# Kernel tuning notes

Measured on AMD Instinct MI355X. Metric: run time of the kernel, lower is better.

The kernel has to match this reference:

```python
import jax, jax.numpy as jnp
from jax import lax
import numpy as np

B = 256
EMB_DIM = 64
N_EMB = 512
LAT1 = 1024   # 16 slots * 64
LAT2 = 512
LAT = LAT1 + LAT2  # 1536
COMMIT = 0.25
EMB_COST = 1.0


def setup_inputs() -> dict:
    key = jax.random.key(0)
    ks = iter(jax.random.split(key, 40))

    def w(shape, fan_in):
        return jax.random.normal(next(ks), shape, jnp.float32) * np.float32(1.0 / np.sqrt(fan_in))

    def b(n):
        return jax.random.normal(next(ks), (n,), jnp.float32) * np.float32(0.01)

    inp = {}
    inp['x'] = jax.random.normal(next(ks), (B, 3, 64, 64), jnp.float32)
    # encoder convs, torch OIHW layout, k=4
    inp['ew0'] = w((64, 3, 4, 4), 3 * 16);   inp['eb0'] = b(64)
    inp['ew1'] = w((64, 64, 4, 4), 64 * 16); inp['eb1'] = b(64)
    inp['ew2'] = w((128, 64, 4, 4), 64 * 16); inp['eb2'] = b(128)
    inp['ew3'] = w((256, 128, 4, 4), 128 * 16); inp['eb3'] = b(256)
    # encoder fc11: 4096 -> 1024 -> 1024 -> 1536, stored (in,out)
    inp['fw0'] = w((4096, 1024), 4096); inp['fb0'] = b(1024)
    inp['fw1'] = w((1024, 1024), 1024); inp['fb1'] = b(1024)
    inp['fw2'] = w((1024, LAT), 1024);  inp['fb2'] = b(LAT)
    # VQ codebook
    inp['codebook'] = jax.random.normal(next(ks), (N_EMB, EMB_DIM), jnp.float32)
    # decoder fc3: 1536 -> 512 -> 1024 -> 4096
    inp['gw0'] = w((LAT, 512), LAT);    inp['gb0'] = b(512)
    inp['gw1'] = w((512, 1024), 512);   inp['gb1'] = b(1024)
    inp['gw2'] = w((1024, 4096), 1024); inp['gb2'] = b(4096)
    # decoder ConvTranspose2d weights, torch layout (Cin, Cout, kh, kw)
    inp['tw0'] = w((256, 128, 4, 4), 256 * 16); inp['tb0'] = b(128)
    inp['tw1'] = w((128, 64, 4, 4), 128 * 16);  inp['tb1'] = b(64)
    inp['tw2'] = w((64, 64, 4, 4), 64 * 16);    inp['tb2'] = b(64)
    inp['tw3'] = w((64, 3, 4, 4), 64 * 16);     inp['tb3'] = b(3)
    return inp


def _conv(x, w, b):
    # Conv2d k=4 s=2 p=1 -> halves H,W
    y = lax.conv_general_dilated(x, w, (2, 2), ((1, 1), (1, 1)),
                                 dimension_numbers=('NCHW', 'OIHW', 'NCHW'))
    return y + b[None, :, None, None]


def _convt(x, w, b):
    # ConvTranspose2d k=4 s=2 p=1 -> doubles H,W.
    # Equivalent to lhs_dilation=2, pad k-1-p=2, flipped kernel, swapped I/O.
    wf = jnp.flip(w, (2, 3)).transpose(1, 0, 2, 3)
    y = lax.conv_general_dilated(x, wf, (1, 1), ((2, 2), (2, 2)),
                                 lhs_dilation=(2, 2),
                                 dimension_numbers=('NCHW', 'OIHW', 'NCHW'))
    return y + b[None, :, None, None]


def _forward(x, ew0, eb0, ew1, eb1, ew2, eb2, ew3, eb3,
             fw0, fb0, fw1, fb1, fw2, fb2, codebook,
             gw0, gb0, gw1, gb1, gw2, gb2,
             tw0, tb0, tw1, tb1, tw2, tb2, tw3, tb3):
    relu = jax.nn.relu
    # --- encoder conv stack (last conv has no ReLU) ---
    h = relu(_conv(x, ew0, eb0))
    h = relu(_conv(h, ew1, eb1))
    h = relu(_conv(h, ew2, eb2))
    h = _conv(h, ew3, eb3)                      # [B,256,4,4]
    h = h.reshape(h.shape[0], -1)               # [B,4096]
    h = relu(h @ fw0 + fb0)
    h = relu(h @ fw1 + fb1)
    z = h @ fw2 + fb2                           # [B,1536]
    # --- split content / style (isVQStyle=False) ---
    z_c = z[:, :LAT1]
    z_s = z[:, LAT1:]
    # --- vector quantize z_c (16 slots of dim 64, shared codebook) ---
    flat = z_c.reshape(-1, EMB_DIM)             # [B*16, 64]
    d = (jnp.sum(flat * flat, axis=1, keepdims=True)
         + jnp.sum(codebook * codebook, axis=1)
         - 2.0 * flat @ codebook.T)             # [B*16, 512]
    idx = jnp.argmin(d, axis=1)
    quantized = codebook[idx].reshape(z_c.shape)  # [B,1024]
    sg = lax.stop_gradient
    q_latent_loss = jnp.mean((quantized - sg(z_c)) ** 2) * EMB_COST
    e_latent_loss = jnp.mean((z_c - sg(quantized)) ** 2) * COMMIT
    loss = q_latent_loss + e_latent_loss
    quantized = z_c + sg(quantized - z_c)       # straight-through
    e = jnp.concatenate([quantized, z_s], axis=-1)  # [B,1536]
    # --- decoder ---
    g = relu(e @ gw0 + gb0)
    g = relu(g @ gw1 + gb1)
    g = (g @ gw2 + gb2).reshape(-1, 256, 4, 4)
    g = relu(_convt(g, tw0, tb0))
    g = relu(_convt(g, tw1, tb1))
    g = relu(_convt(g, tw2, tb2))
    x_recon = _convt(g, tw3, tb3)               # [B,3,64,64]
    return x_recon, loss


def reference(x, ew0, eb0, ew1, eb1, ew2, eb2, ew3, eb3,
              fw0, fb0, fw1, fb1, fw2, fb2, codebook,
              gw0, gb0, gw1, gb1, gw2, gb2,
              tw0, tb0, tw1, tb1, tw2, tb2, tw3, tb3):
    return _forward(x, ew0, eb0, ew1, eb1, ew2, eb2, ew3, eb3,
                    fw0, fb0, fw1, fb1, fw2, fb2, codebook,
                    gw0, gb0, gw1, gb1, gw2, gb2,
                    tw0, tb0, tw1, tb1, tw2, tb2, tw3, tb3)
```

## Files before the change

kernel.cpp:

```cpp
#include <hip/hip_runtime.h>
#include <hip/hip_bf16.h>


#define TPB 256
typedef __attribute__((ext_vector_type(8))) short short8v;
typedef __attribute__((ext_vector_type(4))) float f32x4;
typedef unsigned int u32;
typedef unsigned short u16;

__device__ inline u16 f2bf(float x){
  union { __hip_bfloat16 b; u16 u; } cv;
  cv.b = __float2bfloat16(x);
  return cv.u;
}
__device__ inline float bf2f(u16 h){ union{u32 u;float f;}v; v.u=((u32)h)<<16; return v.f;}

template<int NS>
__device__ inline void splitN(float x, u16 t[3]) {
  u16 h0 = f2bf(x); t[0] = h0;
  float r1 = x - bf2f(h0);
  u16 h1 = f2bf(r1); t[1] = h1;
  if (NS == 3) { float r2 = r1 - bf2f(h1); t[2] = f2bf(r2); }
}

template<int NS, int ST>
__device__ inline void stW(u32* L, int row, int oct, const u16 hs[3][8]) {
  constexpr int SWM = (ST == 64) ? 15 : 7;
  const int sw = row & SWM;
#pragma unroll
  for (int s = 0; s < NS; ++s) {
    uint4 d;
    d.x = (u32)hs[s][0] | ((u32)hs[s][1] << 16);
    d.y = (u32)hs[s][2] | ((u32)hs[s][3] << 16);
    d.z = (u32)hs[s][4] | ((u32)hs[s][5] << 16);
    d.w = (u32)hs[s][6] | ((u32)hs[s][7] << 16);
    int ch = (((s << 2) | oct) ^ sw) << 2;
    *reinterpret_cast<uint4*>(&L[row * ST + ch]) = d;
  }
}

template<int NS, int ST>
__device__ inline void stWf(u32* L, int row, int oct, const float v[8]) {
  u16 hs[3][8];
#pragma unroll
  for (int e = 0; e < 8; ++e) {
    u16 t3[3]; splitN<(NS == 3) ? 3 : 2>(v[e], t3);
    hs[0][e] = t3[0]; hs[1][e] = t3[1]; if (NS == 3) hs[2][e] = t3[2];
  }
  stW<NS, ST>(L, row, oct, hs);
}

template<int ST>
__device__ inline void stWp(u32* L, int row, int oct, int s, uint4 d) {
  constexpr int SWM = (ST == 64) ? 15 : 7;
  int ch = (((s << 2) | oct) ^ (row & SWM)) << 2;
  *reinterpret_cast<uint4*>(&L[row * ST + ch]) = d;
}

template<int ST>
__device__ inline short8v rdFrag(const u32* L, int row, int c) {
  constexpr int SWM = (ST == 64) ? 15 : 7;
  int ph = (c ^ (row & SWM)) << 2;
  return *reinterpret_cast<const short8v*>(&L[row * ST + ph]);
}

__global__ __launch_bounds__(TPB) void wsplit3_k(
    const float* __restrict__ src, u16* __restrict__ dst, int n)
{
  for (int i = blockIdx.x * TPB + threadIdx.x; i < n; i += gridDim.x * TPB) {
    u16 t3[3]; splitN<3>(src[i], t3);
    dst[i] = t3[0]; dst[i + n] = t3[1]; dst[i + 2 * n] = t3[2];
  }
}
__global__ __launch_bounds__(TPB) void wprep1_k(
    const float* __restrict__ src, u16* __restrict__ dh, int Ci, int Co)
{
  int K4 = Ci << 2;
  int tot = 4 * Co * K4;
  for (int i = blockIdx.x * TPB + threadIdx.x; i < tot; i += gridDim.x * TPB) {
    int par = i / (Co * K4); int rem = i - par * (Co * K4);
    int co = rem / K4; int k4 = rem - co * K4;
    int ci = k4 >> 2, ay = (k4 >> 1) & 1, ax = k4 & 1;
    int py = par >> 1, px = par & 1;
    int widx = ((1 - py) << 2) + (1 - px) + (ay << 3) + (ax << 1);
    dh[i] = f2bf(src[(((size_t)ci * Co + co) << 4) + widx]);
  }
}

__global__ __launch_bounds__(TPB) void x_pad_k(
    const float* __restrict__ x, float* __restrict__ xp)
{
  int idx = blockIdx.x * TPB + threadIdx.x;
  if (idx >= 3345408) return;
  int px = idx % 66; int t = idx / 66; int py = t % 66; int p = t / 66;
  float v = 0.f;
  if (py >= 1 && py <= 64 && px >= 1 && px <= 64)
    v = x[(size_t)p * 4096 + (py - 1) * 64 + (px - 1)];
  xp[idx] = v;
}
__global__ __launch_bounds__(TPB) void zb0_k(float* __restrict__ h0p)
{
  int idx = blockIdx.x * TPB + threadIdx.x;
  if (idx >= 2162688) return;
  int p = idx / 132, k = idx % 132;
  int py, px;
  if (k < 34)       { py = 0;           px = k; }
  else if (k < 68)  { py = 33;          px = k - 34; }
  else if (k < 100) { py = k - 68 + 1;  px = 0; }
  else              { py = k - 100 + 1; px = 33; }
  h0p[(size_t)p * 1156 + py * 34 + px] = 0.f;
}

template<int RM, int OUTM>
__global__ __launch_bounds__(TPB, 2) void conv_ad(
    const float* __restrict__ in, const u16* __restrict__ wsp,
    const float* __restrict__ bias, float* __restrict__ outp,
    int Ci, int Co, int Wi, int lwo, int relu, int KSPL, int PS,
    int bS, int ciS, int Mtot)
{
  constexpr int BM = RM * 64;
  __shared__ __align__(16) u32 BL[2][64 * 64];
  const int K = Ci << 4;
  const int PW = Wi + 2;
  const int Wo = Wi >> 1;
  const int tid = threadIdx.x;
  const int m0 = blockIdx.x * BM, n0 = blockIdx.y << 6;
  const int lane = tid & 63, wv = tid >> 6, r = lane & 15, g = lane >> 4;
  const int kb0 = blockIdx.z * KSPL;
  const int kbN = min(kb0 + KSPL, K);
  const int khsel = g & 1;
  const int cig = g >> 1;
  f32x4 acc[RM][4] = {};

  int base[RM];
#pragma unroll
  for (int mm = 0; mm < RM; ++mm) {
    int cell = m0 + (wv * RM + mm) * 16 + r;
    int x = cell & (Wo - 1), y = (cell >> lwo) & (Wo - 1), b = cell >> (lwo + lwo);
    base[mm] = b * bS + (2 * y + 2 * khsel) * PW + 2 * x;
  }

  auto gA = [&](int kb, float v[RM][8]) {
    if ((kb + (g << 3)) < K) {
      int cioff = ((kb >> 4) + cig) * ciS;
#pragma unroll
      for (int mm = 0; mm < RM; ++mm) {
        const float* p = in + base[mm] + cioff;
#pragma unroll
        for (int e = 0; e < 8; ++e)
          v[mm][e] = p[(e >> 2) * PW + (e & 3)];
      }
    } else {
#pragma unroll
      for (int mm = 0; mm < RM; ++mm)
#pragma unroll
        for (int e = 0; e < 8; ++e) v[mm][e] = 0.f;
    }
  };
  auto gB = [&](int kb, uint4* d) {
    int n = tid & 63, oc2 = tid >> 6;
    int k8 = kb + (oc2 << 3);
    if (k8 < K) {
      const u16* wp = wsp + (size_t)(n0 + n) * K + k8;
      d[0] = *reinterpret_cast<const uint4*>(wp);
      d[1] = *reinterpret_cast<const uint4*>(wp + PS);
      d[2] = *reinterpret_cast<const uint4*>(wp + 2 * PS);
    } else {
      d[0] = d[1] = d[2] = make_uint4(0u, 0u, 0u, 0u);
    }
  };
  auto mkfrags = [&](const float v[8], short8v f[3]) {
    u16 hs[3][8];
#pragma unroll
    for (int e = 0; e < 8; ++e) {
      u16 t3[3]; splitN<3>(v[e], t3);
      hs[0][e] = t3[0]; hs[1][e] = t3[1]; hs[2][e] = t3[2];
    }
#pragma unroll
    for (int s = 0; s < 3; ++s) {
      union { u16 u[8]; short8v sv; } cv;
#pragma unroll
      for (int e = 0; e < 8; ++e) cv.u[e] = hs[s][e];
      f[s] = cv.sv;
    }
  };

  float vA[RM][8], vA2[RM][8];
  uint4 vB[3], vB2[3];
  gA(kb0, vA); gB(kb0, vB);
  for (int kb = kb0; kb < kbN; kb += 32) {
    u32* BLc = BL[((kb - kb0) >> 5) & 1];
    {
      int n = tid & 63, oc2 = tid >> 6;
      stWp<64>(BLc, n, oc2, 0, vB[0]);
      stWp<64>(BLc, n, oc2, 1, vB[1]);
      stWp<64>(BLc, n, oc2, 2, vB[2]);
    }
    const bool more = (kb + 32) < kbN;
    if (more) { gB(kb + 32, vB2); gA(kb + 32, vA2); }
    short8v a_[RM][3];
#pragma unroll
    for (int mm = 0; mm < RM; ++mm) mkfrags(vA[mm], a_[mm]);
    __syncthreads();
#pragma unroll
    for (int ns = 0; ns < 4; ++ns) {
      short8v b_[3];
#pragma unroll
      for (int s = 0; s < 3; ++s) b_[s] = rdFrag<64>(BLc, (ns << 4) + r, (s << 2) | g);
#pragma unroll
      for (int mm = 0; mm < RM; ++mm) {
        acc[mm][ns] = __builtin_amdgcn_mfma_f32_16x16x32_bf16(a_[mm][0], b_[0], acc[mm][ns], 0, 0, 0);
        acc[mm][ns] = __builtin_amdgcn_mfma_f32_16x16x32_bf16(a_[mm][0], b_[1], acc[mm][ns], 0, 0, 0);
        acc[mm][ns] = __builtin_amdgcn_mfma_f32_16x16x32_bf16(a_[mm][1], b_[0], acc[mm][ns], 0, 0, 0);
        acc[mm][ns] = __builtin_amdgcn_mfma_f32_16x16x32_bf16(a_[mm][1], b_[1], acc[mm][ns], 0, 0, 0);
        acc[mm][ns] = __builtin_amdgcn_mfma_f32_16x16x32_bf16(a_[mm][0], b_[2], acc[mm][ns], 0, 0, 0);
        acc[mm][ns] = __builtin_amdgcn_mfma_f32_16x16x32_bf16(a_[mm][2], b_[0], acc[mm][ns], 0, 0, 0);
      }
    }
    if (more) {
#pragma unroll
      for (int mm = 0; mm < RM; ++mm)
#pragma unroll
        for (int e = 0; e < 8; ++e) vA[mm][e] = vA2[mm][e];
#pragma unroll
      for (int s = 0; s < 3; ++s) vB[s] = vB2[s];
    }
  }
#pragma unroll
  for (int mm = 0; mm < RM; ++mm)
#pragma unroll
    for (int ns = 0; ns < 4; ++ns) {
      int c0 = m0 + (wv * RM + mm) * 16 + (g << 2);
      int co = n0 + (ns << 4) + r;
      if (OUTM == 0) {
        float bv = bias[co];
        const int OPW = Wo + 2;
        const int OPHW = OPW * OPW;
#pragma unroll
        for (int q = 0; q < 4; ++q) {
          int cell = c0 + q;
          int x = cell & (Wo - 1), y = (cell >> lwo) & (Wo - 1), b = cell >> (lwo + lwo);
          float v = acc[mm][ns][q] + bv;
          if (relu) v = fmaxf(v, 0.f);
          outp[((size_t)(b * Co + co)) * OPHW + (y + 1) * OPW + (x + 1)] = v;
        }
      } else {
        float4 o;
        o.x = acc[mm][ns][0]; o.y = acc[mm][ns][1];
        o.z = acc[mm][ns][2]; o.w = acc[mm][ns][3];
        *reinterpret_cast<float4*>(
            &outp[((size_t)(blockIdx.z * Co + co)) * Mtot + c0]) = o;
      }
    }
}

__global__ __launch_bounds__(TPB) void combine_cm_k(
    const float* __restrict__ P, const float* __restrict__ bias,
    float* __restrict__ out)
{
  int idx = blockIdx.x * TPB + threadIdx.x;
  if (idx >= 5308416) return;
  int px = idx % 18; int t = idx / 18; int py = t % 18; t /= 18;
  int b = t % 256; int co = t / 256;
  float v = 0.f;
  if (py >= 1 && py <= 16 && px >= 1 && px <= 16) {
    int cell = b * 256 + (py - 1) * 16 + (px - 1);
    v = P[(size_t)co * 65536 + cell] + P[(size_t)(64 + co) * 65536 + cell] + bias[co];
    v = fmaxf(v, 0.f);
  }
  out[idx] = v;
}

__global__ __launch_bounds__(TPB) void combine_pad_k(
    const float* __restrict__ P, const float* __restrict__ bias,
    float* __restrict__ out)
{
  int idx = blockIdx.x * TPB + threadIdx.x;
  if (idx >= 3276800) return;
  int px = idx % 10; int t = idx / 10; int py = t % 10; t /= 10;
  int co = t % 128; int b = t / 128;
  float v = 0.f;
  if (py >= 1 && py <= 8 && px >= 1 && px <= 8) {
    int cell = b * 64 + (py - 1) * 8 + (px - 1);
    float s = 0.f;
#pragma unroll
    for (int z = 0; z < 4; ++z)
      s += P[((size_t)(z * 128 + co)) * 16384 + cell];
    v = fmaxf(s + bias[co], 0.f);
  }
  out[idx] = v;
}

__global__ __launch_bounds__(TPB) void conv_combine(
    const float* __restrict__ P, const float* __restrict__ bias,
    float* __restrict__ out, int Mtot, int N, int SK, int lwo, int relu)
{
  int idx = blockIdx.x * TPB + threadIdx.x;
  int mq = Mtot >> 2;
  int co = idx / mq;
  int cell0 = (idx - co * mq) << 2;
  if (co >= N) return;
  float4 s = make_float4(0.f, 0.f, 0.f, 0.f);
  for (int z = 0; z < SK; ++z) {
    const float4 pv = *reinterpret_cast<const float4*>(
        &P[((size_t)z * N + co) * Mtot + cell0]);
    s.x += pv.x; s.y += pv.y; s.z += pv.z; s.w += pv.w;
  }
  float bv = bias[co];
  s.x += bv; s.y += bv; s.z += bv; s.w += bv;
  if (relu) { s.x = fmaxf(s.x, 0.f); s.y = fmaxf(s.y, 0.f);
              s.z = fmaxf(s.z, 0.f); s.w = fmaxf(s.w, 0.f); }
  int Wo = 1 << lwo;
  int x = cell0 & (Wo - 1), y = (cell0 >> lwo) & (Wo - 1), b = cell0 >> (lwo + lwo);
  *reinterpret_cast<float4*>(&out[(((size_t)b * N + co) * Wo + y) * Wo + x]) = s;
}

template<int NS, int OUTM>
__global__ __launch_bounds__(TPB) void gemm_mf(
    const float* __restrict__ A, const float* __restrict__ W,
    const float* __restrict__ bias, void* __restrict__ outp,
    int M, int K, int N, int KSPL)
{
  constexpr int ST = (NS == 3) ? 64 : 32;
  __shared__ __align__(16) u32 L[(64 + 64) * ST];
  u32* AL = L; u32* BL = L + 64 * ST;
  const int tid = threadIdx.x;
  const int m0 = blockIdx.x << 6, n0 = blockIdx.y << 6;
  const int lane = tid & 63, wv = tid >> 6, r = lane & 15, g = lane >> 4;
  const int kb0 = blockIdx.z * KSPL;
  const int kbN = kb0 + KSPL;
  const int cl = tid & 63, oct = tid >> 6;
  f32x4 acc[4] = {};

  float vA[8], vB[8], vA2[8], vB2[8];
  auto gA = [&](int kt, float* v) {
    const float* ap = &A[(size_t)(m0 + cl) * K + kt + (oct << 3)];
    *reinterpret_cast<float4*>(&v[0]) = *reinterpret_cast<const float4*>(ap);
    *reinterpret_cast<float4*>(&v[4]) = *reinterpret_cast<const float4*>(ap + 4);
  };
  auto gB = [&](int kt, float* v) {
#pragma unroll
    for (int e = 0; e < 8; ++e)
      v[e] = W[(size_t)(kt + (oct << 3) + e) * N + n0 + cl];
  };

  gA(kb0, vA); gB(kb0, vB);
  for (int kt = kb0; kt < kbN; kt += 32) {
    const bool more = (kt + 32) < kbN;
    if (more) { gA(kt + 32, vA2); gB(kt + 32, vB2); }
    stWf<NS, ST>(AL, cl, oct, vA);
    stWf<NS, ST>(BL, cl, oct, vB);
    __syncthreads();
    short8v a_[3];
#pragma unroll
    for (int s = 0; s < NS; ++s) a_[s] = rdFrag<ST>(AL, (wv << 4) + r, (s << 2) | g);
#pragma unroll
    for (int ns = 0; ns < 4; ++ns) {
      short8v b_[3];
#pragma unroll
      for (int s = 0; s < NS; ++s) b_[s] = rdFrag<ST>(BL, (ns << 4) + r, (s << 2) | g);
      acc[ns] = __builtin_amdgcn_mfma_f32_16x16x32_bf16(a_[0], b_[0], acc[ns], 0, 0, 0);
      if (NS >= 2) {
        acc[ns] = __builtin_amdgcn_mfma_f32_16x16x32_bf16(a_[0], b_[1], acc[ns], 0, 0, 0);
        acc[ns] = __builtin_amdgcn_mfma_f32_16x16x32_bf16(a_[1], b_[0], acc[ns], 0, 0, 0);
      }
      if (NS == 3) {
        acc[ns] = __builtin_amdgcn_mfma_f32_16x16x32_bf16(a_[1], b_[1], acc[ns], 0, 0, 0);
        acc[ns] = __builtin_amdgcn_mfma_f32_16x16x32_bf16(a_[0], b_[2], acc[ns], 0, 0, 0);
        acc[ns] = __builtin_amdgcn_mfma_f32_16x16x32_bf16(a_[2], b_[0], acc[ns], 0, 0, 0);
      }
    }
    __syncthreads();
    if (more) {
#pragma unroll
      for (int e = 0; e < 8; ++e) { vA[e] = vA2[e]; vB[e] = vB2[e]; }
    }
  }
#pragma unroll
  for (int ns = 0; ns < 4; ++ns)
#pragma unroll
    for (int q = 0; q < 4; ++q) {
      int m = m0 + (wv << 4) + (g << 2) + q;
      int n = n0 + (ns << 4) + r;
      float v = acc[ns][q];
      if (OUTM == 0) ((float*)outp)[((size_t)blockIdx.z * M + m) * N + n] = v;
      else           ((u32*)outp)[(size_t)m * N + n] = (u32)f2bf(v + bias[n]);
    }
}

__global__ __launch_bounds__(TPB) void combine_k(
    const float* __restrict__ P, const float* __restrict__ bias,
    float* __restrict__ out, int MN, int N, int SK, int relu)
{
  int i4 = (blockIdx.x * TPB + threadIdx.x) << 2;
  if (i4 >= MN) return;
  float4 s = make_float4(0.f, 0.f, 0.f, 0.f);
  for (int z = 0; z < SK; ++z) {
    const float4 pv = *reinterpret_cast<const float4*>(&P[(size_t)z * MN + i4]);
    s.x += pv.x; s.y += pv.y; s.z += pv.z; s.w += pv.w;
  }
  int n = i4 % N;
  s.x += bias[n]; s.y += bias[n + 1]; s.z += bias[n + 2]; s.w += bias[n + 3];
  if (relu) { s.x = fmaxf(s.x, 0.f); s.y = fmaxf(s.y, 0.f);
              s.z = fmaxf(s.z, 0.f); s.w = fmaxf(s.w, 0.f); }
  *reinterpret_cast<float4*>(&out[i4]) = s;
}

__global__ __launch_bounds__(TPB) void combine_pk_k(
    const float* __restrict__ P, const float* __restrict__ bias,
    u32* __restrict__ out)
{
  int i4 = (blockIdx.x * TPB + threadIdx.x) << 2;
  if (i4 >= 1048576) return;
  const float4 p0 = *reinterpret_cast<const float4*>(&P[i4]);
  const float4 p1 = *reinterpret_cast<const float4*>(&P[1048576 + i4]);
  int n = i4 % 4096;
  uint4 o;
  o.x = (u32)f2bf(p0.x + p1.x + bias[n]);
  o.y = (u32)f2bf(p0.y + p1.y + bias[n + 1]);
  o.z = (u32)f2bf(p0.z + p1.z + bias[n + 2]);
  o.w = (u32)f2bf(p0.w + p1.w + bias[n + 3]);
  *reinterpret_cast<uint4*>(&out[i4]) = o;
}

template<int RM, int EMIT, int SPLITIN>
__global__ __launch_bounds__(TPB) void convt_ad(
    const u32* __restrict__ in, const u16* __restrict__ wth,
    const float* __restrict__ bias, u32* __restrict__ outq,
    int Ci, int Co, int Hi, int lwi, int relu)
{
  constexpr int BM = RM * 64;
  constexpr int STC = BM + 4;
  constexpr int LB = 2 * 64 * 32;
  constexpr int LSZ = (LB > 16 * STC) ? LB : 16 * STC;
  __shared__ __align__(16) u32 L[LSZ];
  const int Wi = Hi, K4 = Ci << 2;
  const int HW = Hi * Wi, HWq = HW >> 2, Wiq = Wi >> 1;
  const int par = blockIdx.z, py = par >> 1, px = par & 1;
  const int tid = threadIdx.x;
  const int m0 = blockIdx.x * BM, n0 = blockIdx.y << 6;
  const int lane = tid & 63, wv = tid >> 6, r = lane & 15, g = lane >> 4;
  const int stepCi = SPLITIN ? HWq : HW;
  f32x4 acc[RM][4] = {};

  int offT[RM][4]; u32 mskT[RM][4];
#pragma unroll
  for (int mm = 0; mm < RM; ++mm) {
    int cell = m0 + (wv * RM + mm) * 16 + r;
    int X = cell & (Wi - 1), Y = (cell >> lwi) & (Wi - 1), b = cell >> (lwi + lwi);
#pragma unroll
    for (int t = 0; t < 4; ++t) {
      int ay = t >> 1, ax = t & 1;
      int gy = Y + py - ay, gx = X + px - ax;
      bool ok = (gy >= 0 && gy < Hi && gx >= 0 && gx < Wi);
      int gyc = min(max(gy, 0), Hi - 1), gxc = min(max(gx, 0), Wi - 1);
      if (SPLITIN) {
        int q = ((gyc & 1) << 1) | (gxc & 1);
        offT[mm][t] = q * (256 * Ci * HWq) + b * Ci * HWq + (gyc >> 1) * Wiq + (gxc >> 1);
      } else {
        offT[mm][t] = b * Ci * HW + gyc * Wi + gxc;
      }
      mskT[mm][t] = ok ? 0xffffffffu : 0u;
    }
  }

  auto gA = [&](int kb, u32 v[RM][8]) {
    int cib = ((kb >> 2) + (g << 1)) * stepCi;
#pragma unroll
    for (int mm = 0; mm < RM; ++mm)
#pragma unroll
      for (int e = 0; e < 8; ++e) {
        int t = e & 3;
        v[mm][e] = in[offT[mm][t] + cib + ((e >> 2) ? stepCi : 0)] & mskT[mm][t];
      }
  };
  auto gB = [&](int kb, uint4* d) {
    int n = tid & 63, oc2 = tid >> 6;
    *d = *reinterpret_cast<const uint4*>(
        wth + (size_t)(par * Co + n0 + n) * K4 + kb + (oc2 << 3));
  };

  u32 vA[RM][8], vA2[RM][8];
  uint4 vB, vB2;
  gA(0, vA); gB(0, &vB);
  int cur = 0;
  for (int kb = 0; kb < K4; kb += 32) {
    u32* BLc = L + cur * (64 * 32);
    {
      int n = tid & 63, oc2 = tid >> 6;
      stWp<32>(BLc, n, oc2, 0, vB);
    }
    const bool more = (kb + 32) < K4;
    if (more) { gB(kb + 32, &vB2); gA(kb + 32, vA2); }
    short8v a_[RM];
#pragma unroll
    for (int mm = 0; mm < RM; ++mm) {
      const u32* v = vA[mm];
      union { uint4 u; short8v s; } ch;
      ch.u.x = (v[0] & 0xffffu) | (v[1] << 16);
      ch.u.y = (v[2] & 0xffffu) | (v[3] << 16);
      ch.u.z = (v[4] & 0xffffu) | (v[5] << 16);
      ch.u.w = (v[6] & 0xffffu) | (v[7] << 16);
      a_[mm] = ch.s;
    }
    __syncthreads();
#pragma unroll
    for (int ns = 0; ns < 4; ++ns) {
      short8v b0 = rdFrag<32>(BLc, (ns << 4) + r, g);
#pragma unroll
      for (int mm = 0; mm < RM; ++mm)
        acc[mm][ns] = __builtin_amdgcn_mfma_f32_16x16x32_bf16(a_[mm], b0, acc[mm][ns], 0, 0, 0);
    }
    if (more) {
#pragma unroll
      for (int mm = 0; mm < RM; ++mm)
#pragma unroll
        for (int e = 0; e < 8; ++e) vA[mm][e] = vA2[mm][e];
      vB = vB2;
    }
    cur ^= 1;
  }
  const size_t QO = (size_t)256 * Co * HW;
  u32* op = outq + (size_t)par * QO;
  constexpr int C4N = BM / 4;
#pragma unroll
  for (int ph = 0; ph < 4; ++ph) {
    __syncthreads();
    float bv = bias[n0 + (ph << 4) + r];
#pragma unroll
    for (int mm = 0; mm < RM; ++mm)
#pragma unroll
      for (int q = 0; q < 4; ++q) {
        int cell = (wv * RM + mm) * 16 + (g << 2) + q;
        float v = acc[mm][ph][q] + bv;
        if (relu) v = fmaxf(v, 0.f);
        L[r * STC + cell] = EMIT ? (u32)f2bf(v) : __float_as_uint(v);
      }
    __syncthreads();
#pragma unroll
    for (int it = 0; it < RM; ++it) {
      int lin = it * TPB + tid;
      int c4 = lin & (C4N - 1);
      int colL = lin / C4N;
      int col = (ph << 4) + colL;
      int cell0 = c4 << 2;
      uint4 d = *reinterpret_cast<const uint4*>(&L[colL * STC + cell0]);
      int gc = m0 + cell0;
      int Xo = gc & (Wi - 1), Yo = (gc >> lwi) & (Wi - 1), bo = gc >> (lwi + lwi);
      *reinterpret_cast<uint4*>(
          &op[((size_t)(bo * Co + n0 + col) * Hi + Yo) * Wi + Xo]) = d;
    }
  }
}

__global__ __launch_bounds__(TPB) void convt3_kernel(
    const float* __restrict__ inq, const float* __restrict__ w,
    float* __restrict__ part)
{
  __shared__ float wl[3072];
  __shared__ float il[8][33 * 32];
  const int b = blockIdx.x;
  const int z = blockIdx.y;
  const int tid = threadIdx.x;
  for (int i = tid; i < 3072; i += TPB) wl[i] = w[i];
  const int Y = tid >> 3;
  const int X0 = (tid & 7) << 2;
  float acc[3][2][8];
#pragma unroll
  for (int o = 0; o < 3; ++o)
#pragma unroll
    for (int p = 0; p < 2; ++p)
#pragma unroll
      for (int q = 0; q < 8; ++q) acc[o][p][q] = 0.f;

  const int cbeg = z << 5, cend = cbeg + 32;
  for (int c0 = cbeg; c0 < cend; c0 += 8) {
    __syncthreads();
    for (int i = tid; i < 8192; i += TPB) {
      int cc = i >> 10, yy = (i >> 5) & 31, xx = i & 31;
      int q = ((yy & 1) << 1) | (xx & 1);
      il[cc][yy * 33 + xx] = inq[(size_t)q * 4194304 +
          (((size_t)b * 64 + c0 + cc) * 16 + (yy >> 1)) * 16 + (xx >> 1)];
    }
    __syncthreads();
    for (int cc = 0; cc < 8; ++cc) {
      float iv[3][6];
#pragma unroll
      for (int j = 0; j < 3; ++j) {
        int gy = Y - 1 + j;
        int gyc = min(max(gy, 0), 31);
        float my = (gy >= 0 && gy < 32) ? 1.f : 0.f;
#pragma unroll
        for (int k = 0; k < 6; ++k) {
          int gx = X0 - 1 + k;
          int gxc = min(max(gx, 0), 31);
          float mx = (gx >= 0 && gx < 32) ? 1.f : 0.f;
          iv[j][k] = il[cc][gyc * 33 + gxc] * (my * mx);
        }
      }
      const float* wq = &wl[(c0 + cc) * 48];
#pragma unroll
      for (int o = 0; o < 3; ++o) {
        const float* wo = wq + o * 16;
#pragma unroll
        for (int c = 0; c < 4; ++c) {
          acc[o][0][2*c]   = fmaf(iv[1][c+1], wo[5],  acc[o][0][2*c]);
          acc[o][0][2*c]   = fmaf(iv[1][c],   wo[7],  acc[o][0][2*c]);
          acc[o][0][2*c]   = fmaf(iv[0][c+1], wo[13], acc[o][0][2*c]);
          acc[o][0][2*c]   = fmaf(iv[0][c],   wo[15], acc[o][0][2*c]);
          acc[o][0][2*c+1] = fmaf(iv[1][c+2], wo[4],  acc[o][0][2*c+1]);
          acc[o][0][2*c+1] = fmaf(iv[1][c+1], wo[6],  acc[o][0][2*c+1]);
          acc[o][0][2*c+1] = fmaf(iv[0][c+2], wo[12], acc[o][0][2*c+1]);
          acc[o][0][2*c+1] = fmaf(iv[0][c+1], wo[14], acc[o][0][2*c+1]);
          acc[o][1][2*c]   = fmaf(iv[2][c+1], wo[1],  acc[o][1][2*c]);
          acc[o][1][2*c]   = fmaf(iv[2][c],   wo[3],  acc[o][1][2*c]);
          acc[o][1][2*c]   = fmaf(iv[1][c+1], wo[9],  acc[o][1][2*c]);
          acc[o][1][2*c]   = fmaf(iv[1][c],   wo[11], acc[o][1][2*c]);
          acc[o][1][2*c+1] = fmaf(iv[2][c+2], wo[0],  acc[o][1][2*c+1]);
          acc[o][1][2*c+1] = fmaf(iv[2][c+1], wo[2],  acc[o][1][2*c+1]);
          acc[o][1][2*c+1] = fmaf(iv[1][c+2], wo[8],  acc[o][1][2*c+1]);
          acc[o][1][2*c+1] = fmaf(iv[1][c+1], wo[10], acc[o][1][2*c+1]);
        }
      }
    }
  }
  float* pz = part + (size_t)z * 3145728;
#pragma unroll
  for (int o = 0; o < 3; ++o) {
#pragma unroll
    for (int p = 0; p < 2; ++p) {
      float* op = pz + (((size_t)b * 3 + o) * 64 + 2 * Y + p) * 64 + 2 * X0;
      *reinterpret_cast<float4*>(op) =
          make_float4(acc[o][p][0], acc[o][p][1], acc[o][p][2], acc[o][p][3]);
      *reinterpret_cast<float4*>(op + 4) =
          make_float4(acc[o][p][4], acc[o][p][5], acc[o][p][6], acc[o][p][7]);
    }
  }
}

__global__ __launch_bounds__(TPB) void c3_combine(
    const float* __restrict__ part, const float* __restrict__ bias,
    float* __restrict__ out)
{
  int i4 = (blockIdx.x * TPB + threadIdx.x) << 2;
  const float4 p0 = *reinterpret_cast<const float4*>(&part[i4]);
  const float4 p1 = *reinterpret_cast<const float4*>(&part[i4 + 3145728]);
  int o = (i4 >> 12) % 3;
  float bv = bias[o];
  float4 s = make_float4(p0.x + p1.x + bv, p0.y + p1.y + bv,
                         p0.z + p1.z + bv, p0.w + p1.w + bv);
  *reinterpret_cast<float4*>(&out[i4]) = s;
}

__global__ __launch_bounds__(TPB) void vq8_kernel(
    const float* __restrict__ z, const float* __restrict__ cb,
    float* __restrict__ e, float* __restrict__ rowloss)
{
  __shared__ float cbL[64][65];
  __shared__ float zr[8][64];
  const int tid = threadIdx.x;
  const int lane = tid & 63, wid = tid >> 6;
  const int r0 = blockIdx.x << 3;

  for (int i = tid; i < 512; i += TPB) {
    int rr = i >> 6, k = i & 63;
    int row = r0 + rr;
    int b = row >> 4, s = row & 15;
    zr[rr][k] = z[(size_t)b * 1536 + s * 64 + k];
  }

  float best[2] = {3.4e38f, 3.4e38f};
  int bi[2] = {0, 0};

  for (int c0 = 0; c0 < 512; c0 += 64) {
    __syncthreads();
#pragma unroll
    for (int i = 0; i < 4; ++i) {
      int j = (tid >> 4) + (i << 4);
      int kq = tid & 15;
      const float4 v = *reinterpret_cast<const float4*>(
          &cb[(size_t)(c0 + j) * 64 + (kq << 2)]);
      cbL[(kq << 2) + 0][j] = v.x;
      cbL[(kq << 2) + 1][j] = v.y;
      cbL[(kq << 2) + 2][j] = v.z;
      cbL[(kq << 2) + 3][j] = v.w;
    }
    __syncthreads();
#pragma unroll
    for (int rep = 0; rep < 2; ++rep) {
      const float* zp = zr[wid + (rep << 2)];
      float d = 0.f;
#pragma unroll
      for (int k = 0; k < 64; ++k) {
        float t = zp[k] - cbL[k][lane];
        d = fmaf(t, t, d);
      }
      if (d < best[rep]) { best[rep] = d; bi[rep] = c0 + lane; }
    }
  }
#pragma unroll
  for (int rep = 0; rep < 2; ++rep) {
#pragma unroll
    for (int off = 32; off > 0; off >>= 1) {
      float ob = __shfl_xor(best[rep], off);
      int   oi = __shfl_xor(bi[rep], off);
      if (ob < best[rep] || (ob == best[rep] && oi < bi[rep])) {
        best[rep] = ob; bi[rep] = oi;
      }
    }
    int row = r0 + wid + (rep << 2);
    int b = row >> 4, s = row & 15;
    e[(size_t)b * 1536 + s * 64 + lane] = cb[(size_t)bi[rep] * 64 + lane];
    if (lane == 0) rowloss[row] = best[rep];
  }
}

__global__ __launch_bounds__(TPB) void zs_copy_kernel(
    const float* __restrict__ z, float* __restrict__ e)
{
  int i = blockIdx.x * TPB + threadIdx.x;
  int b = i >> 9, k = i & 511;
  e[(size_t)b * 1536 + 1024 + k] = z[(size_t)b * 1536 + 1024 + k];
}

__global__ __launch_bounds__(TPB) void loss_reduce_kernel(
    const float* __restrict__ rl, float* __restrict__ out)
{
  __shared__ float sm[TPB];
  float s = 0.f;
  for (int i = threadIdx.x; i < 4096; i += TPB) s += rl[i];
  sm[threadIdx.x] = s;
  __syncthreads();
  for (int sft = 128; sft > 0; sft >>= 1) {
    if (threadIdx.x < sft) sm[threadIdx.x] += sm[threadIdx.x + sft];
    __syncthreads();
  }
  if (threadIdx.x == 0) out[0] = sm[0] * (1.25f / 262144.f);
}

extern "C" void kernel_launch(void* const* d_in, const int* in_sizes, int n_in,
                              void* d_out, int out_size, void* d_ws, size_t ws_size,
                              hipStream_t stream)
{
  const float* x    = (const float*)d_in[0];
  const float* ew0  = (const float*)d_in[1];
  const float* eb0  = (const float*)d_in[2];
  const float* ew1  = (const float*)d_in[3];
  const float* eb1  = (const float*)d_in[4];
  const float* ew2  = (const float*)d_in[5];
  const float* eb2  = (const float*)d_in[6];
  const float* ew3  = (const float*)d_in[7];
  const float* eb3  = (const float*)d_in[8];
  const float* fw0  = (const float*)d_in[9];
  const float* fb0  = (const float*)d_in[10];
  const float* fw1  = (const float*)d_in[11];
  const float* fb1  = (const float*)d_in[12];
  const float* fw2  = (const float*)d_in[13];
  const float* fb2  = (const float*)d_in[14];
  const float* cb   = (const float*)d_in[15];
  const float* gw0  = (const float*)d_in[16];
  const float* gb0  = (const float*)d_in[17];
  const float* gw1  = (const float*)d_in[18];
  const float* gb1  = (const float*)d_in[19];
  const float* gw2  = (const float*)d_in[20];
  const float* gb2  = (const float*)d_in[21];
  const float* tw0  = (const float*)d_in[22];
  const float* tb0  = (const float*)d_in[23];
  const float* tw1  = (const float*)d_in[24];
  const float* tb1  = (const float*)d_in[25];
  const float* tw2  = (const float*)d_in[26];
  const float* tb2  = (const float*)d_in[27];
  const float* tw3  = (const float*)d_in[28];
  const float* tb3  = (const float*)d_in[29];

  float* out = (float*)d_out;
  float* ws  = (float*)d_ws;

  u16*   WE0  = (u16*)(ws + 0);
  u16*   WE1  = (u16*)(ws + 4608);
  u16*   WE2  = (u16*)(ws + 102912);
  u16*   WE3  = (u16*)(ws + 299520);
  float* RL   = ws + 1085952;
  float* H0P  = ws + 1090048;
  float* PC1  = ws + 20029952;
  float* XP   = ws + 20029952;
  float* H1P  = ws + 1090048;
  float* PC23 = ws + 6398464;
  float* H2P  = ws + 14787072;
  float* H3   = ws + 18063872;
  float* P    = ws + 1090048;
  float* F0   = ws + 5284352;
  float* F1   = ws + 5546496;
  float* Z    = ws + 5808640;
  float* E    = ws + 6201856;
  float* G0   = ws + 6595072;
  float* G1   = ws + 6726144;
  float* T2S  = ws + 1090048;
  u16*   WT0h = (u16*)(ws + 17867264);
  u16*   WT1h = (u16*)(ws + 18391552);
  u16*   WT2h = (u16*)(ws + 18522624);
  float* PG2  = ws + 18588160;
  u32*   G2P  = (u32*)(ws + 20685312);
  u32*   T0S  = (u32*)(ws + 21733888);
  u32*   T1S  = (u32*)(ws + 23831040);
  float* PT3  = ws + 18588160;

  wsplit3_k<<<dim3(12),  TPB, 0, stream>>>(ew0, WE0, 3072);
  wsplit3_k<<<dim3(256), TPB, 0, stream>>>(ew1, WE1, 65536);
  wsplit3_k<<<dim3(512), TPB, 0, stream>>>(ew2, WE2, 131072);
  wsplit3_k<<<dim3(1024),TPB, 0, stream>>>(ew3, WE3, 524288);
  x_pad_k<<<dim3(13068), TPB, 0, stream>>>(x, XP);
  zb0_k<<<dim3(8448), TPB, 0, stream>>>(H0P);

  conv_ad<4,0><<<dim3(1024, 1, 1), TPB, 0, stream>>>(
      XP, WE0, eb0, H0P, 3, 64, 64, 5, 1, 48, 3072, 13068, 4356, 0);
  conv_ad<4,1><<<dim3(256, 1, 2), TPB, 0, stream>>>(
      H0P, WE1, eb1, PC1, 64, 64, 32, 4, 1, 512, 65536, 73984, 1156, 65536);
  combine_cm_k<<<dim3(20736), TPB, 0, stream>>>(PC1, eb1, H1P);
  conv_ad<4,1><<<dim3(64, 2, 4), TPB, 0, stream>>>(
      H1P, WE2, eb2, PC23, 64, 128, 16, 3, 1, 256, 131072, 324, 82944, 16384);
  combine_pad_k<<<dim3(12800), TPB, 0, stream>>>(PC23, eb2, H2P);
  conv_ad<4,1><<<dim3(16, 4, 8), TPB, 0, stream>>>(
      H2P, WE3, eb3, PC23, 128, 256, 8, 2, 0, 256, 524288, 12800, 100, 4096);
  conv_combine<<<dim3(1024), TPB, 0, stream>>>(PC23, eb3, H3, 4096, 256, 8, 2, 0);

  gemm_mf<3,0><<<dim3(4, 16, 16), TPB, 0, stream>>>(H3, fw0, fb0, (void*)P, 256, 4096, 1024, 256);
  combine_k<<<dim3(256), TPB, 0, stream>>>(P, fb0, F0, 262144, 1024, 16, 1);
  gemm_mf<3,0><<<dim3(4, 16, 8), TPB, 0, stream>>>(F0, fw1, fb1, (void*)P, 256, 1024, 1024, 128);
  combine_k<<<dim3(256), TPB, 0, stream>>>(P, fb1, F1, 262144, 1024, 8, 1);
  gemm_mf<3,0><<<dim3(4, 24, 8), TPB, 0, stream>>>(F1, fw2, fb2, (void*)P, 256, 1024, 1536, 128);
  combine_k<<<dim3(384), TPB, 0, stream>>>(P, fb2, Z, 393216, 1536, 8, 0);

  vq8_kernel<<<dim3(512), TPB, 0, stream>>>(Z, cb, E, RL);
  zs_copy_kernel<<<dim3(512), TPB, 0, stream>>>(Z, E);
  loss_reduce_kernel<<<dim3(1), TPB, 0, stream>>>(RL, out + (size_t)out_size - 1);

  gemm_mf<2,0><<<dim3(4, 8, 8), TPB, 0, stream>>>(E,  gw0, gb0, (void*)P, 256, 1536, 512, 192);
  combine_k<<<dim3(128), TPB, 0, stream>>>(P, gb0, G0, 131072, 512, 8, 1);
  gemm_mf<2,0><<<dim3(4, 16, 4), TPB, 0, stream>>>(G0, gw1, gb1, (void*)P, 256, 512, 1024, 128);
  combine_k<<<dim3(256), TPB, 0, stream>>>(P, gb1, G1, 262144, 1024, 4, 1);

  wprep1_k<<<dim3(512), TPB, 0, stream>>>(tw0, WT0h, 256, 128);
  wprep1_k<<<dim3(128), TPB, 0, stream>>>(tw1, WT1h, 128, 64);
  wprep1_k<<<dim3(64),  TPB, 0, stream>>>(tw2, WT2h, 64, 64);

  gemm_mf<1,0><<<dim3(4, 64, 2), TPB, 0, stream>>>(G1, gw2, gb2, (void*)PG2, 256, 1024, 4096, 512);
  combine_pk_k<<<dim3(1024), TPB, 0, stream>>>(PG2, gb2, G2P);

  convt_ad<2,1,0><<<dim3(32, 2, 4),  TPB, 0, stream>>>(G2P, WT0h, tb0, T0S, 256, 128, 4,  2, 1);
  convt_ad<2,1,1><<<dim3(128, 1, 4), TPB, 0, stream>>>(T0S, WT1h, tb1, T1S, 128, 64,  8,  3, 1);
  convt_ad<2,0,1><<<dim3(512, 1, 4), TPB, 0, stream>>>(T1S, WT2h, tb2, (u32*)T2S, 64, 64, 16, 4, 1);
  convt3_kernel<<<dim3(256, 2), TPB, 0, stream>>>(T2S, tw3, PT3);
  c3_combine<<<dim3(3072), TPB, 0, stream>>>(PT3, tb3, out);
}
```

Baseline: 508.8 us.

## Merge prep kernels, fold z_s copy into VQ, emit bf16 for last convT

Several small launches are merged: the encoder weight splits become one kernel, input padding and halo zeroing become one, decoder weight prep becomes one, and the z_s copy moves into the VQ kernel. The third transposed conv now writes packed bf16 instead of fp32, and the final convT reads bf16, which halves that intermediate's traffic. This cuts launch overhead and memory bandwidth, but the final layer's input loses precision compared with fp32. The EMIT=0 path now stores bf16-converted values in LDS even though it writes u32, so it can change results.

```diff
diff --git a/kernel.cpp b/kernel.cpp
--- a/kernel.cpp
+++ b/kernel.cpp
@@ -64,51 +64,67 @@
   return *reinterpret_cast<const short8v*>(&L[row * ST + ph]);
 }
 
-__global__ __launch_bounds__(TPB) void wsplit3_k(
-    const float* __restrict__ src, u16* __restrict__ dst, int n)
-{
-  for (int i = blockIdx.x * TPB + threadIdx.x; i < n; i += gridDim.x * TPB) {
-    u16 t3[3]; splitN<3>(src[i], t3);
-    dst[i] = t3[0]; dst[i + n] = t3[1]; dst[i + 2 * n] = t3[2];
-  }
-}
-__global__ __launch_bounds__(TPB) void wprep1_k(
-    const float* __restrict__ src, u16* __restrict__ dh, int Ci, int Co)
-{
+__device__ inline u16 wprep1_elem(const float* __restrict__ src, int i,
+                                  int Ci, int Co) {
   int K4 = Ci << 2;
-  int tot = 4 * Co * K4;
-  for (int i = blockIdx.x * TPB + threadIdx.x; i < tot; i += gridDim.x * TPB) {
-    int par = i / (Co * K4); int rem = i - par * (Co * K4);
-    int co = rem / K4; int k4 = rem - co * K4;
-    int ci = k4 >> 2, ay = (k4 >> 1) & 1, ax = k4 & 1;
-    int py = par >> 1, px = par & 1;
-    int widx = ((1 - py) << 2) + (1 - px) + (ay << 3) + (ax << 1);
-    dh[i] = f2bf(src[(((size_t)ci * Co + co) << 4) + widx]);
-  }
-}
-
-__global__ __launch_bounds__(TPB) void x_pad_k(
-    const float* __restrict__ x, float* __restrict__ xp)
+  int par = i / (Co * K4); int rem = i - par * (Co * K4);
+  int co = rem / K4; int k4 = rem - co * K4;
+  int ci = k4 >> 2, ay = (k4 >> 1) & 1, ax = k4 & 1;
+  int py = par >> 1, px = par & 1;
+  int widx = ((1 - py) << 2) + (1 - px) + (ay << 3) + (ax << 1);
+  return f2bf(src[(((size_t)ci * Co + co) << 4) + widx]);
+}
+__device__ inline void wsplit3_elem(const float* __restrict__ src,
+                                    u16* __restrict__ dst, int i, int n) {
+  u16 t3[3]; splitN<3>(src[i], t3);
+  dst[i] = t3[0]; dst[i + n] = t3[1]; dst[i + 2 * n] = t3[2];
+}
+
+__global__ __launch_bounds__(TPB) void prep_enc_k(
+    const float* __restrict__ ew0, const float* __restrict__ ew1,
+    const float* __restrict__ ew2, const float* __restrict__ ew3,
+    u16* __restrict__ WE0, u16* __restrict__ WE1,
+    u16* __restrict__ WE2, u16* __restrict__ WE3)
 {
   int idx = blockIdx.x * TPB + threadIdx.x;
-  if (idx >= 3345408) return;
-  int px = idx % 66; int t = idx / 66; int py = t % 66; int p = t / 66;
-  float v = 0.f;
-  if (py >= 1 && py <= 64 && px >= 1 && px <= 64)
-    v = x[(size_t)p * 4096 + (py - 1) * 64 + (px - 1)];
-  xp[idx] = v;
-}
-__global__ __launch_bounds__(TPB) void zb0_k(float* __restrict__ h0p)
+  if (idx < 3072)     { wsplit3_elem(ew0, WE0, idx, 3072); return; }
+  if (idx < 68608)    { wsplit3_elem(ew1, WE1, idx - 3072, 65536); return; }
+  if (idx < 199680)   { wsplit3_elem(ew2, WE2, idx - 68608, 131072); return; }
+  if (idx < 723968)   { wsplit3_elem(ew3, WE3, idx - 199680, 524288); return; }
+}
+
+__global__ __launch_bounds__(TPB) void prep_dec_k(
+    const float* __restrict__ tw0, const float* __restrict__ tw1,
+    const float* __restrict__ tw2,
+    u16* __restrict__ WT0, u16* __restrict__ WT1, u16* __restrict__ WT2)
 {
   int idx = blockIdx.x * TPB + threadIdx.x;
-  if (idx >= 2162688) return;
-  int p = idx / 132, k = idx % 132;
-  int py, px;
-  if (k < 34)       { py = 0;           px = k; }
-  else if (k < 68)  { py = 33;          px = k - 34; }
-  else if (k < 100) { py = k - 68 + 1;  px = 0; }
-  else              { py = k - 100 + 1; px = 33; }
-  h0p[(size_t)p * 1156 + py * 34 + px] = 0.f;
+  if (idx < 524288)   { WT0[idx] = wprep1_elem(tw0, idx, 256, 128); return; }
+  if (idx < 655360)   { WT1[idx - 524288] = wprep1_elem(tw1, idx - 524288, 128, 64); return; }
+  if (idx < 720896)   { WT2[idx - 655360] = wprep1_elem(tw2, idx - 655360, 64, 64); return; }
+}
+
+__global__ __launch_bounds__(TPB) void prep_inp_k(
+    const float* __restrict__ x, float* __restrict__ xp,
+    float* __restrict__ h0p)
+{
+  int idx = blockIdx.x * TPB + threadIdx.x;
+  if (idx < 3345408) {
+    int px = idx % 66; int t = idx / 66; int py = t % 66; int p = t / 66;
+    float v = 0.f;
+    if (py >= 1 && py <= 64 && px >= 1 && px <= 64)
+      v = x[(size_t)p * 4096 + (py - 1) * 64 + (px - 1)];
+    xp[idx] = v;
+  } else if (idx < 5508096) {
+    int i2 = idx - 3345408;
+    int p = i2 / 132, k = i2 % 132;
+    int py, px;
+    if (k < 34)       { py = 0;           px = k; }
+    else if (k < 68)  { py = 33;          px = k - 34; }
+    else if (k < 100) { py = k - 68 + 1;  px = 0; }
+    else              { py = k - 100 + 1; px = 33; }
+    h0p[(size_t)p * 1156 + py * 34 + px] = 0.f;
+  }
 }
 
 template<int RM, int OUTM>
@@ -521,7 +537,6 @@
     cur ^= 1;
   }
   const size_t QO = (size_t)256 * Co * HW;
-  u32* op = outq + (size_t)par * QO;
   constexpr int C4N = BM / 4;
 #pragma unroll
   for (int ph = 0; ph < 4; ++ph) {
@@ -534,27 +549,52 @@
         int cell = (wv * RM + mm) * 16 + (g << 2) + q;
         float v = acc[mm][ph][q] + bv;
         if (relu) v = fmaxf(v, 0.f);
-        L[r * STC + cell] = EMIT ? (u32)f2bf(v) : __float_as_uint(v);
-      }
-    __syncthreads();
-#pragma unroll
-    for (int it = 0; it < RM; ++it) {
-      int lin = it * TPB + tid;
-      int c4 = lin & (C4N - 1);
-      int colL = lin / C4N;
-      int col = (ph << 4) + colL;
-      int cell0 = c4 << 2;
-      uint4 d = *reinterpret_cast<const uint4*>(&L[colL * STC + cell0]);
-      int gc = m0 + cell0;
-      int Xo = gc & (Wi - 1), Yo = (gc >> lwi) & (Wi - 1), bo = gc >> (lwi + lwi);
-      *reinterpret_cast<uint4*>(
-          &op[((size_t)(bo * Co + n0 + col) * Hi + Yo) * Wi + Xo]) = d;
+        L[r * STC + cell] = (u32)f2bf(v);
+      }
+    __syncthreads();
+    if (EMIT == 2) {
+      u16* op16 = (u16*)outq + (size_t)par * QO;
+      constexpr int C8N = BM / 8;
+      constexpr int NIT = (BM * 16) / (TPB * 8);
+#pragma unroll
+      for (int it = 0; it < NIT; ++it) {
+        int lin = it * TPB + tid;
+        int c8 = lin & (C8N - 1);
+        int colL = lin / C8N;
+        int col = (ph << 4) + colL;
+        int cell0 = c8 << 3;
+        const u32* lp = &L[colL * STC + cell0];
+        uint4 d;
+        d.x = (lp[0] & 0xffffu) | (lp[1] << 16);
+        d.y = (lp[2] & 0xffffu) | (lp[3] << 16);
+        d.z = (lp[4] & 0xffffu) | (lp[5] << 16);
+        d.w = (lp[6] & 0xffffu) | (lp[7] << 16);
+        int gc = m0 + cell0;
+        int Xo = gc & (Wi - 1), Yo = (gc >> lwi) & (Wi - 1), bo = gc >> (lwi + lwi);
+        *reinterpret_cast<uint4*>(
+            &op16[((size_t)(bo * Co + n0 + col) * Hi + Yo) * Wi + Xo]) = d;
+      }
+    } else {
+      u32* op = outq + (size_t)par * QO;
+#pragma unroll
+      for (int it = 0; it < RM; ++it) {
+        int lin = it * TPB + tid;
+        int c4 = lin & (C4N - 1);
+        int colL = lin / C4N;
+        int col = (ph << 4) + colL;
+        int cell0 = c4 << 2;
+        uint4 d = *reinterpret_cast<const uint4*>(&L[colL * STC + cell0]);
+        int gc = m0 + cell0;
+        int Xo = gc & (Wi - 1), Yo = (gc >> lwi) & (Wi - 1), bo = gc >> (lwi + lwi);
+        *reinterpret_cast<uint4*>(
+            &op[((size_t)(bo * Co + n0 + col) * Hi + Yo) * Wi + Xo]) = d;
+      }
     }
   }
 }
 
 __global__ __launch_bounds__(TPB) void convt3_kernel(
-    const float* __restrict__ inq, const float* __restrict__ w,
+    const u16* __restrict__ inq, const float* __restrict__ w,
     float* __restrict__ part)
 {
   __shared__ float wl[3072];
@@ -579,8 +619,8 @@
     for (int i = tid; i < 8192; i += TPB) {
       int cc = i >> 10, yy = (i >> 5) & 31, xx = i & 31;
       int q = ((yy & 1) << 1) | (xx & 1);
-      il[cc][yy * 33 + xx] = inq[(size_t)q * 4194304 +
-          (((size_t)b * 64 + c0 + cc) * 16 + (yy >> 1)) * 16 + (xx >> 1)];
+      il[cc][yy * 33 + xx] = bf2f(inq[(size_t)q * 4194304 +
+          (((size_t)b * 64 + c0 + cc) * 16 + (yy >> 1)) * 16 + (xx >> 1)]);
     }
     __syncthreads();
     for (int cc = 0; cc < 8; ++cc) {
@@ -668,6 +708,12 @@
     int b = row >> 4, s = row & 15;
     zr[rr][k] = z[(size_t)b * 1536 + s * 64 + k];
   }
+  {
+    int b = r0 >> 4;
+    int half = (r0 >> 3) & 1;
+    size_t o = (size_t)b * 1536 + 1024 + half * 256 + tid;
+    e[o] = z[o];
+  }
 
   float best[2] = {3.4e38f, 3.4e38f};
   int bi[2] = {0, 0};
@@ -713,14 +759,6 @@
     e[(size_t)b * 1536 + s * 64 + lane] = cb[(size_t)bi[rep] * 64 + lane];
     if (lane == 0) rowloss[row] = best[rep];
   }
-}
-
-__global__ __launch_bounds__(TPB) void zs_copy_kernel(
-    const float* __restrict__ z, float* __restrict__ e)
-{
-  int i = blockIdx.x * TPB + threadIdx.x;
-  int b = i >> 9, k = i & 511;
-  e[(size_t)b * 1536 + 1024 + k] = z[(size_t)b * 1536 + 1024 + k];
 }
 
 __global__ __launch_bounds__(TPB) void loss_reduce_kernel(
@@ -795,7 +833,7 @@
   float* E    = ws + 6201856;
   float* G0   = ws + 6595072;
   float* G1   = ws + 6726144;
-  float* T2S  = ws + 1090048;
+  u16*   T2S16= (u16*)(ws + 1090048);
   u16*   WT0h = (u16*)(ws + 17867264);
   u16*   WT1h = (u16*)(ws + 18391552);
   u16*   WT2h = (u16*)(ws + 18522624);
@@ -805,12 +843,9 @@
   u32*   T1S  = (u32*)(ws + 23831040);
   float* PT3  = ws + 18588160;
 
-  wsplit3_k<<<dim3(12),  TPB, 0, stream>>>(ew0, WE0, 3072);
-  wsplit3_k<<<dim3(256), TPB, 0, stream>>>(ew1, WE1, 65536);
-  wsplit3_k<<<dim3(512), TPB, 0, stream>>>(ew2, WE2, 131072);
-  wsplit3_k<<<dim3(1024),TPB, 0, stream>>>(ew3, WE3, 524288);
-  x_pad_k<<<dim3(13068), TPB, 0, stream>>>(x, XP);
-  zb0_k<<<dim3(8448), TPB, 0, stream>>>(H0P);
+  prep_enc_k<<<dim3(2828), TPB, 0, stream>>>(
+      ew0, ew1, ew2, ew3, WE0, WE1, WE2, WE3);
+  prep_inp_k<<<dim3(21516), TPB, 0, stream>>>(x, XP, H0P);
 
   conv_ad<4,0><<<dim3(1024, 1, 1), TPB, 0, stream>>>(
       XP, WE0, eb0, H0P, 3, 64, 64, 5, 1, 48, 3072, 13068, 4356, 0);
@@ -831,8 +866,9 @@
   gemm_mf<3,0><<<dim3(4, 24, 8), TPB, 0, stream>>>(F1, fw2, fb2, (void*)P, 256, 1024, 1536, 128);
   combine_k<<<dim3(384), TPB, 0, stream>>>(P, fb2, Z, 393216, 1536, 8, 0);
 
+  prep_dec_k<<<dim3(2816), TPB, 0, stream>>>(tw0, tw1, tw2, WT0h, WT1h, WT2h);
+
   vq8_kernel<<<dim3(512), TPB, 0, stream>>>(Z, cb, E, RL);
-  zs_copy_kernel<<<dim3(512), TPB, 0, stream>>>(Z, E);
   loss_reduce_kernel<<<dim3(1), TPB, 0, stream>>>(RL, out + (size_t)out_size - 1);
 
   gemm_mf<2,0><<<dim3(4, 8, 8), TPB, 0, stream>>>(E,  gw0, gb0, (void*)P, 256, 1536, 512, 192);
@@ -840,16 +876,12 @@
   gemm_mf<2,0><<<dim3(4, 16, 4), TPB, 0, stream>>>(G0, gw1, gb1, (void*)P, 256, 512, 1024, 128);
   combine_k<<<dim3(256), TPB, 0, stream>>>(P, gb1, G1, 262144, 1024, 4, 1);
 
-  wprep1_k<<<dim3(512), TPB, 0, stream>>>(tw0, WT0h, 256, 128);
-  wprep1_k<<<dim3(128), TPB, 0, stream>>>(tw1, WT1h, 128, 64);
-  wprep1_k<<<dim3(64),  TPB, 0, stream>>>(tw2, WT2h, 64, 64);
-
   gemm_mf<1,0><<<dim3(4, 64, 2), TPB, 0, stream>>>(G1, gw2, gb2, (void*)PG2, 256, 1024, 4096, 512);
   combine_pk_k<<<dim3(1024), TPB, 0, stream>>>(PG2, gb2, G2P);
 
   convt_ad<2,1,0><<<dim3(32, 2, 4),  TPB, 0, stream>>>(G2P, WT0h, tb0, T0S, 256, 128, 4,  2, 1);
   convt_ad<2,1,1><<<dim3(128, 1, 4), TPB, 0, stream>>>(T0S, WT1h, tb1, T1S, 128, 64,  8,  3, 1);
-  convt_ad<2,0,1><<<dim3(512, 1, 4), TPB, 0, stream>>>(T1S, WT2h, tb2, (u32*)T2S, 64, 64, 16, 4, 1);
-  convt3_kernel<<<dim3(256, 2), TPB, 0, stream>>>(T2S, tw3, PT3);
+  convt_ad<2,2,1><<<dim3(512, 1, 4), TPB, 0, stream>>>(T1S, WT2h, tb2, (u32*)T2S16, 64, 64, 16, 4, 1);
+  convt3_kernel<<<dim3(256, 2), TPB, 0, stream>>>(T2S16, tw3, PT3);
   c3_combine<<<dim3(3072), TPB, 0, stream>>>(PT3, tb3, out);
 }
```

Result: faster. 492.6 us (-3.2%).
